# Kernel optimization log

Measured on AMD Instinct MI355X. Metric: run time of the kernel, lower is better.

Reference implementation:

```python
import jax, jax.numpy as jnp
import numpy as np

BETA = 0.9      # snntorch Leaky decay
THRESH = 1.0    # default threshold
SLOPE = 25.0    # fast_sigmoid surrogate slope

# Heaviside spike with fast_sigmoid surrogate gradient: d/dx = 1/(slope*|x|+1)^2
@jax.custom_vjp
def spike_fn(x):
    return (x > 0).astype(x.dtype)

def _spike_fwd(x):
    return (x > 0).astype(x.dtype), x

def _spike_bwd(x, g):
    return (g / (SLOPE * jnp.abs(x) + 1.0) ** 2,)

spike_fn.defvjp(_spike_fwd, _spike_bwd)

def setup_inputs() -> dict:
    key = jax.random.key(0)
    k0, k1, k2 = jax.random.split(key, 3)
    B, T, F, H, C = 8192, 200, 40, 128, 5
    x = jax.random.normal(k0, (B, T, F), dtype=jnp.float32)
    w1 = jax.random.normal(k1, (H, F), dtype=jnp.float32) / np.sqrt(F).astype(np.float32)
    b1 = jnp.zeros((H,), jnp.float32)
    w2 = jax.random.normal(k2, (C, H), dtype=jnp.float32) / np.sqrt(H).astype(np.float32)
    b2 = jnp.zeros((C,), jnp.float32)
    return {"x": x, "w1": w1, "b1": b1, "w2": w2, "b2": b2}

def reference(x, w1, b1, w2, b2):
    # x: [B, T, F] -> time-major [T, B, F] (matches x.permute(1,0,2))
    xt = jnp.transpose(x, (1, 0, 2))
    B = x.shape[0]
    mem1 = jnp.zeros((B, w1.shape[0]), x.dtype)
    mem2 = jnp.zeros((B, w2.shape[0]), x.dtype)

    def step(carry, x_t):
        m1, m2 = carry
        cur1 = x_t @ w1.T + b1                       # [B, 128]
        # snntorch Leaky, reset_mechanism='subtract'; reset is detached
        reset1 = jax.lax.stop_gradient((m1 > THRESH).astype(x_t.dtype))
        m1 = BETA * m1 + cur1 - reset1 * THRESH
        spk1 = spike_fn(m1 - THRESH)
        cur2 = spk1 @ w2.T + b2                      # [B, 5]
        reset2 = jax.lax.stop_gradient((m2 > THRESH).astype(x_t.dtype))
        m2 = BETA * m2 + cur2 - reset2 * THRESH
        spk2 = spike_fn(m2 - THRESH)
        return (m1, m2), spk2

    _, spk2_rec = jax.lax.scan(step, (mem1, mem2), xt)
    return spk2_rec  # [T, B, 5], like torch.stack(spk2_rec, dim=0)
```

## Files before the change

kernel.cpp:

```cpp
#include <hip/hip_runtime.h>
#include <cstdint>

#define T_STEPS 200
#define B_TOTAL 8192
#define F_IN    40
#define H_DIM   128
#define C_OUT   5

#define CH      8
#define NCHUNK  (T_STEPS / CH)
#define CHB     (CH * F_IN * 4)
#define WIN     2048
#define ROWB    (T_STEPS * F_IN * 4)

typedef float v2f __attribute__((ext_vector_type(2)));
typedef float v4f __attribute__((ext_vector_type(4)));

#define PKFMA_LO(acc, xp, wp)                                                  \
    asm("v_pk_fma_f32 %0, %1, %2, %0 op_sel:[0,0,0] op_sel_hi:[0,1,1]"        \
        : "+v"(acc) : "v"(xp), "v"(wp))
#define PKFMA_HI(acc, xp, wp)                                                  \
    asm("v_pk_fma_f32 %0, %1, %2, %0 op_sel:[1,0,0] op_sel_hi:[1,1,1]"        \
        : "+v"(acc) : "v"(xp), "v"(wp))

__device__ __forceinline__ void gload_lds16(const void* g, void* l) {
    __builtin_amdgcn_global_load_lds(
        (const __attribute__((address_space(1))) void*)g,
        (__attribute__((address_space(3))) void*)l, 16, 0, 0);
}

__global__ __launch_bounds__(256, 2)
void snn_l1(const float* __restrict__ x,
            const float* __restrict__ w1,
            const float* __restrict__ b1,
            ulonglong2* __restrict__ masks)
{
    __shared__ __align__(16) char xs[2][4][WIN];

    const int li = threadIdx.x & 63;
    const int wv = threadIdx.x >> 6;
    const int b  = blockIdx.x * 4 + wv;
    const int hA = li, hB = li + 64;

    v2f wab[F_IN];
    {
        const float* wArow = w1 + hA * F_IN;
        const float* wBrow = w1 + hB * F_IN;
#pragma unroll
        for (int f = 0; f < F_IN; ++f) {
            v2f p; p.x = wArow[f]; p.y = wBrow[f];
            wab[f] = p;
        }
    }
    const float b1A = b1[hA], b1B = b1[hB];
    float mA = 0.0f, mB = 0.0f, rA = 0.0f, rB = 0.0f;

    const char* xb = (const char*)x + (size_t)b * ROWB + (size_t)li * 16;

    auto winstart = [](int c) { return (c == NCHUNK - 1) ? (ROWB - WIN) : c * CHB; };

    gload_lds16(xb + winstart(0),        &xs[0][wv][0]);
    gload_lds16(xb + winstart(0) + 1024, &xs[0][wv][1024]);
    asm volatile("s_waitcnt vmcnt(0)" ::: "memory");

    ulonglong2* mp = masks + b;

    for (int c = 0; c < NCHUNK; ++c) {
        if (c + 1 < NCHUNK) {
            const int ws = winstart(c + 1);
            gload_lds16(xb + ws,        &xs[(c + 1) & 1][wv][0]);
            gload_lds16(xb + ws + 1024, &xs[(c + 1) & 1][wv][1024]);
        }
        const int delta = c * CHB - winstart(c);
        const char* xsw = &xs[c & 1][wv][0];

#pragma unroll
        for (int s = 0; s < CH; ++s) {
            const v4f* xrow = (const v4f*)(xsw + delta + s * (F_IN * 4));
            v2f acc = {0.0f, 0.0f};
#pragma unroll
            for (int q = 0; q < 10; ++q) {
                const v4f xq = xrow[q];
                const v2f xlo = xq.lo, xhi = xq.hi;
                PKFMA_LO(acc, xlo, wab[4*q+0]);
                PKFMA_HI(acc, xlo, wab[4*q+1]);
                PKFMA_LO(acc, xhi, wab[4*q+2]);
                PKFMA_HI(acc, xhi, wab[4*q+3]);
            }
            mA = __fsub_rn(__fadd_rn(__fmul_rn(0.9f, mA), __fadd_rn(acc.x, b1A)), rA);
            mB = __fsub_rn(__fadd_rn(__fmul_rn(0.9f, mB), __fadd_rn(acc.y, b1B)), rB);
            const bool sA = mA > 1.0f;
            const bool sB = mB > 1.0f;
            rA = sA ? 1.0f : 0.0f;
            rB = sB ? 1.0f : 0.0f;
            const unsigned long long lo = __ballot(sA);
            const unsigned long long hi = __ballot(sB);
            if (li == 0) *mp = make_ulonglong2(lo, hi);
            mp += B_TOTAL;
        }
        asm volatile("s_waitcnt vmcnt(0)" ::: "memory");
    }
}

__global__ __launch_bounds__(256)
void snn_l2a(const ulonglong2* __restrict__ masks,
             const float* __restrict__ w2,
             float* __restrict__ cur2)
{
    __shared__ float w2s[H_DIM * C_OUT];
    const int tid = threadIdx.x;
    for (int i = tid; i < H_DIM * C_OUT; i += 256) {
        const int c = i / H_DIM, h = i % H_DIM;
        w2s[h * C_OUT + c] = w2[i];
    }
    __syncthreads();

    const size_t gid = (size_t)blockIdx.x * 256 + tid;
    const ulonglong2 mk = masks[gid];
    float s0 = 0.f, s1 = 0.f, s2 = 0.f, s3 = 0.f, s4 = 0.f;

    auto acc32 = [&](uint32_t w, int base) {
        while (w) {
            const int h = base + __builtin_ctz(w);
            w &= w - 1;
            const float* wp = &w2s[h * C_OUT];
            s0 = __fadd_rn(s0, wp[0]);
            s1 = __fadd_rn(s1, wp[1]);
            s2 = __fadd_rn(s2, wp[2]);
            s3 = __fadd_rn(s3, wp[3]);
            s4 = __fadd_rn(s4, wp[4]);
        }
    };
    acc32((uint32_t)(mk.x & 0xffffffffull), 0);
    acc32((uint32_t)(mk.x >> 32), 32);
    acc32((uint32_t)(mk.y & 0xffffffffull), 64);
    acc32((uint32_t)(mk.y >> 32), 96);

    float* o = cur2 + gid * C_OUT;
    o[0] = s0; o[1] = s1; o[2] = s2; o[3] = s3; o[4] = s4;
}

__global__ __launch_bounds__(256)
void snn_l2b(const float* __restrict__ cur2,
             const float* __restrict__ b2,
             float* __restrict__ out)
{
    const int gid = blockIdx.x * 256 + threadIdx.x;
    const float b2c = b2[gid % 5];
    const int STRIDE = B_TOTAL * C_OUT;
    float m2 = 0.0f, r2 = 0.0f;

    float f0 = cur2[0 * (size_t)STRIDE + gid];
    float f1 = cur2[1 * (size_t)STRIDE + gid];
    float f2 = cur2[2 * (size_t)STRIDE + gid];
    float f3 = cur2[3 * (size_t)STRIDE + gid];

#define L2B_STEP(F, TT)                                                        \
    {                                                                          \
        const float cur = __fadd_rn(F, b2c);                                   \
        m2 = __fsub_rn(__fadd_rn(__fmul_rn(0.9f, m2), cur), r2);               \
        const float s = (m2 > 1.0f) ? 1.0f : 0.0f;                             \
        r2 = s;                                                                \
        out[(size_t)(TT) * STRIDE + gid] = s;                                  \
        F = ((TT) + 4 < T_STEPS) ? cur2[(size_t)((TT) + 4) * STRIDE + gid]     \
                                 : 0.0f;                                       \
    }

    for (int t = 0; t < T_STEPS; t += 4) {
        L2B_STEP(f0, t + 0)
        L2B_STEP(f1, t + 1)
        L2B_STEP(f2, t + 2)
        L2B_STEP(f3, t + 3)
    }
#undef L2B_STEP
}

extern "C" void kernel_launch(void* const* d_in, const int* in_sizes, int n_in,
                              void* d_out, int out_size, void* d_ws, size_t ws_size,
                              hipStream_t stream) {
    const float* x  = (const float*)d_in[0];
    const float* w1 = (const float*)d_in[1];
    const float* b1 = (const float*)d_in[2];
    const float* w2 = (const float*)d_in[3];
    const float* b2 = (const float*)d_in[4];
    float* out = (float*)d_out;

    ulonglong2* masks = (ulonglong2*)d_ws;
    float* cur2 = (float*)((char*)d_ws + (size_t)T_STEPS * B_TOTAL * 16);

    snn_l1 <<<dim3(B_TOTAL / 4),             dim3(256), 0, stream>>>(x, w1, b1, masks);
    snn_l2a<<<dim3(T_STEPS * B_TOTAL / 256), dim3(256), 0, stream>>>(masks, w2, cur2);
    snn_l2b<<<dim3(B_TOTAL * C_OUT / 256),   dim3(256), 0, stream>>>(cur2, b2, out);
}
```

Baseline: 295.7 us.

## Split hidden units across waves and pack FMA over timestep pairs

```diff
diff --git a/kernel.cpp b/kernel.cpp
--- a/kernel.cpp
+++ b/kernel.cpp
@@ -14,14 +14,17 @@
 #define ROWB    (T_STEPS * F_IN * 4)
 
 typedef float v2f __attribute__((ext_vector_type(2)));
-typedef float v4f __attribute__((ext_vector_type(4)));
-
-#define PKFMA_LO(acc, xp, wp)                                                  \
-    asm("v_pk_fma_f32 %0, %1, %2, %0 op_sel:[0,0,0] op_sel_hi:[0,1,1]"        \
-        : "+v"(acc) : "v"(xp), "v"(wp))
-#define PKFMA_HI(acc, xp, wp)                                                  \
-    asm("v_pk_fma_f32 %0, %1, %2, %0 op_sel:[1,0,0] op_sel_hi:[1,1,1]"        \
-        : "+v"(acc) : "v"(xp), "v"(wp))
+
+#define DSREAD2(dst, addr, o0, o1)                                             \
+    asm volatile("ds_read2_b32 %0, %1 offset0:%c2 offset1:%c3"                 \
+                 : "=v"(dst) : "v"(addr), "i"(o0), "i"(o1))
+
+#define PKFMA_BW0(acc, xp, wpair)                                              \
+    asm volatile("v_pk_fma_f32 %0, %1, %2, %0 op_sel:[0,0,0] op_sel_hi:[1,0,1]"\
+                 : "+v"(acc) : "v"(xp), "v"(wpair))
+#define PKFMA_BW1(acc, xp, wpair)                                              \
+    asm volatile("v_pk_fma_f32 %0, %1, %2, %0 op_sel:[0,1,0] op_sel_hi:[1,1,1]"\
+                 : "+v"(acc) : "v"(xp), "v"(wpair))
 
 __device__ __forceinline__ void gload_lds16(const void* g, void* l) {
     __builtin_amdgcn_global_load_lds(
@@ -29,31 +32,35 @@
         (__attribute__((address_space(3))) void*)l, 16, 0, 0);
 }
 
+__device__ __forceinline__ unsigned lds_addr(const void* p) {
+    return (unsigned)(uintptr_t)(const __attribute__((address_space(3))) char*)p;
+}
+
 __global__ __launch_bounds__(256, 2)
 void snn_l1(const float* __restrict__ x,
             const float* __restrict__ w1,
             const float* __restrict__ b1,
-            ulonglong2* __restrict__ masks)
+            unsigned long long* __restrict__ masks)
 {
     __shared__ __align__(16) char xs[2][4][WIN];
 
     const int li = threadIdx.x & 63;
     const int wv = threadIdx.x >> 6;
-    const int b  = blockIdx.x * 4 + wv;
-    const int hA = li, hB = li + 64;
-
-    v2f wab[F_IN];
+    const int w  = wv & 1;
+    const int b  = blockIdx.x * 2 + (wv >> 1);
+    const int h  = w * 64 + li;
+
+    v2f wp[F_IN / 2];
     {
-        const float* wArow = w1 + hA * F_IN;
-        const float* wBrow = w1 + hB * F_IN;
-#pragma unroll
-        for (int f = 0; f < F_IN; ++f) {
-            v2f p; p.x = wArow[f]; p.y = wBrow[f];
-            wab[f] = p;
-        }
-    }
-    const float b1A = b1[hA], b1B = b1[hB];
-    float mA = 0.0f, mB = 0.0f, rA = 0.0f, rB = 0.0f;
+        const v2f* wr = (const v2f*)(w1 + h * F_IN);
+#pragma unroll
+        for (int k = 0; k < F_IN / 2; ++k) wp[k] = wr[k];
+    }
+#pragma unroll
+    for (int k = 0; k < F_IN / 2; ++k) asm volatile("" : "+v"(wp[k]));
+
+    const float b1h = b1[h];
+    float m = 0.0f, r = 0.0f;
 
     const char* xb = (const char*)x + (size_t)b * ROWB + (size_t)li * 16;
 
@@ -63,7 +70,7 @@
     gload_lds16(xb + winstart(0) + 1024, &xs[0][wv][1024]);
     asm volatile("s_waitcnt vmcnt(0)" ::: "memory");
 
-    ulonglong2* mp = masks + b;
+    unsigned long long* mp = masks + ((size_t)b * 2 + w);
 
     for (int c = 0; c < NCHUNK; ++c) {
         if (c + 1 < NCHUNK) {
@@ -72,31 +79,44 @@
             gload_lds16(xb + ws + 1024, &xs[(c + 1) & 1][wv][1024]);
         }
         const int delta = c * CHB - winstart(c);
-        const char* xsw = &xs[c & 1][wv][0];
-
-#pragma unroll
-        for (int s = 0; s < CH; ++s) {
-            const v4f* xrow = (const v4f*)(xsw + delta + s * (F_IN * 4));
+        const unsigned lbase = lds_addr(&xs[c & 1][wv][0]) + delta;
+
+#pragma unroll
+        for (int sp = 0; sp < CH / 2; ++sp) {
+            const unsigned a = lbase + sp * 320;
+            v2f xp[8];
             v2f acc = {0.0f, 0.0f};
 #pragma unroll
-            for (int q = 0; q < 10; ++q) {
-                const v4f xq = xrow[q];
-                const v2f xlo = xq.lo, xhi = xq.hi;
-                PKFMA_LO(acc, xlo, wab[4*q+0]);
-                PKFMA_HI(acc, xlo, wab[4*q+1]);
-                PKFMA_LO(acc, xhi, wab[4*q+2]);
-                PKFMA_HI(acc, xhi, wab[4*q+3]);
+            for (int j = 0; j < 8; ++j) DSREAD2(xp[j], a, j, j + F_IN);
+#pragma unroll
+            for (int g = 0; g < 10; ++g) {
+                if (g < 9) asm volatile("s_waitcnt lgkmcnt(4)" ::: "memory");
+                else       asm volatile("s_waitcnt lgkmcnt(0)" ::: "memory");
+                PKFMA_BW0(acc, xp[(4*g + 0) & 7], wp[2*g + 0]);
+                PKFMA_BW1(acc, xp[(4*g + 1) & 7], wp[2*g + 0]);
+                PKFMA_BW0(acc, xp[(4*g + 2) & 7], wp[2*g + 1]);
+                PKFMA_BW1(acc, xp[(4*g + 3) & 7], wp[2*g + 1]);
+                if (g < 8) {
+#pragma unroll
+                    for (int j = 0; j < 4; ++j) {
+                        const int f2 = 4*g + 8 + j;
+                        DSREAD2(xp[f2 & 7], a, f2, f2 + F_IN);
+                    }
+                }
             }
-            mA = __fsub_rn(__fadd_rn(__fmul_rn(0.9f, mA), __fadd_rn(acc.x, b1A)), rA);
-            mB = __fsub_rn(__fadd_rn(__fmul_rn(0.9f, mB), __fadd_rn(acc.y, b1B)), rB);
-            const bool sA = mA > 1.0f;
-            const bool sB = mB > 1.0f;
-            rA = sA ? 1.0f : 0.0f;
-            rB = sB ? 1.0f : 0.0f;
-            const unsigned long long lo = __ballot(sA);
-            const unsigned long long hi = __ballot(sB);
-            if (li == 0) *mp = make_ulonglong2(lo, hi);
-            mp += B_TOTAL;
+            m = __fsub_rn(__fadd_rn(__fmul_rn(0.9f, m), __fadd_rn(acc.x, b1h)), r);
+            bool s0 = m > 1.0f;
+            r = s0 ? 1.0f : 0.0f;
+            unsigned long long bal = __ballot(s0);
+            if (li == 0) *mp = bal;
+            mp += B_TOTAL * 2;
+
+            m = __fsub_rn(__fadd_rn(__fmul_rn(0.9f, m), __fadd_rn(acc.y, b1h)), r);
+            s0 = m > 1.0f;
+            r = s0 ? 1.0f : 0.0f;
+            bal = __ballot(s0);
+            if (li == 0) *mp = bal;
+            mp += B_TOTAL * 2;
         }
         asm volatile("s_waitcnt vmcnt(0)" ::: "memory");
     }
@@ -185,10 +205,10 @@
     const float* b2 = (const float*)d_in[4];
     float* out = (float*)d_out;
 
-    ulonglong2* masks = (ulonglong2*)d_ws;
+    unsigned long long* masks = (unsigned long long*)d_ws;
     float* cur2 = (float*)((char*)d_ws + (size_t)T_STEPS * B_TOTAL * 16);
 
-    snn_l1 <<<dim3(B_TOTAL / 4),             dim3(256), 0, stream>>>(x, w1, b1, masks);
-    snn_l2a<<<dim3(T_STEPS * B_TOTAL / 256), dim3(256), 0, stream>>>(masks, w2, cur2);
+    snn_l1 <<<dim3(B_TOTAL / 2),             dim3(256), 0, stream>>>(x, w1, b1, masks);
+    snn_l2a<<<dim3(T_STEPS * B_TOTAL / 256), dim3(256), 0, stream>>>((const ulonglong2*)masks, w2, cur2);
     snn_l2b<<<dim3(B_TOTAL * C_OUT / 256),   dim3(256), 0, stream>>>(cur2, b2, out);
 }
```

Result: slower. 508.2 us (+71.9%).
